# Optimization experiments

Measured on AMD Instinct MI355X. Metric: run time of the kernel, lower is better.

Reference implementation:

```python
import jax, jax.numpy as jnp
import numpy as np

D_STATE = 8
D_CONV = 4
DT_RANK = 8
THRESHOLD = 0.5
KPOOL = 3
PAD = (KPOOL - 1) // 2
EPS = 1e-5


def _rmsnorm(x, w):
    return x * jax.lax.rsqrt(jnp.mean(x * x, axis=-1, keepdims=True) + EPS) * w


def _dw_causal_conv(x, w, b):
    # x: (L, T, C), w: (C, 1, K) depthwise causal conv along T
    xt = jnp.transpose(x, (0, 2, 1))  # (L, C, T)
    y = jax.lax.conv_general_dilated(
        xt, w, window_strides=(1,), padding=[(D_CONV - 1, 0)],
        dimension_numbers=('NCH', 'OIH', 'NCH'), feature_group_count=xt.shape[1])
    return jnp.transpose(y, (0, 2, 1)) + b


def _selective_scan(x, delta, A, B, Cm, D):
    # x, delta: (L,T,d); A: (d,n); B, Cm: (L,T,n); D: (d,)
    dA = jnp.exp(delta[..., None] * A)                        # (L,T,d,n)
    dBx = (delta * x)[..., None] * B[:, :, None, :]           # (L,T,d,n)
    def combine(a, b):
        a1, b1 = a
        a2, b2 = b
        return (a2 * a1, a2 * b1 + b2)
    _, h = jax.lax.associative_scan(combine, (dA, dBx), axis=1)
    y = jnp.einsum('ltdn,ltn->ltd', h, Cm)
    return y + x * D


def _mamba_block(x, in_proj, conv_w, conv_b, x_proj_w, dt_proj_w, dt_proj_b,
                 A_log_f, A_log_b, D_f, D_b, out_proj_w, rms_w):
    # single-depth bidirectional (bimamba-v2 style) block, expand=1, residual + RMSNorm
    res = x
    xn = _rmsnorm(x, rms_w)
    xz = xn @ in_proj                       # (L,T,2C)
    xi, z = jnp.split(xz, 2, axis=-1)
    xi = jax.nn.silu(_dw_causal_conv(xi, conv_w, conv_b))
    dbl = xi @ x_proj_w                     # (L,T,dt_rank+2*d_state)
    dt = dbl[..., :DT_RANK]
    Bm = dbl[..., DT_RANK:DT_RANK + D_STATE]
    Cm = dbl[..., DT_RANK + D_STATE:]
    delta = jax.nn.softplus(dt @ dt_proj_w + dt_proj_b)
    A_f = -jnp.exp(A_log_f)
    A_b = -jnp.exp(A_log_b)
    flip = lambda a: a[:, ::-1]
    y_f = _selective_scan(xi, delta, A_f, Bm, Cm, D_f)
    y_b = flip(_selective_scan(flip(xi), flip(delta), A_b, flip(Bm), flip(Cm), D_b))
    y = 0.5 * (y_f + y_b) * jax.nn.silu(z)  # if_devide_out -> average two directions
    return res + y @ out_proj_w


def reference(feats, in_proj, conv_w, conv_b, x_proj_w, dt_proj_w, dt_proj_b,
              A_log_f, A_log_b, D_f, D_b, out_proj_w, rms_w, mlp_w, mlp_b,
              record_len):
    N, C, H, W = feats.shape
    T = H * W
    rec = np.asarray(record_len)  # static ragged group sizes
    ends = np.cumsum(rec)
    starts = ends - rec
    masks = []
    for s0, L in zip(starts.tolist(), rec.tolist()):
        g = feats[s0:s0 + L]                       # (L,C,H,W)
        if L > 1:
            x = g.reshape(L, C, T).transpose(0, 2, 1)  # l c h w -> l (h w) c
            feat = _mamba_block(x, in_proj, conv_w, conv_b, x_proj_w, dt_proj_w,
                                dt_proj_b, A_log_f, A_log_b, D_f, D_b,
                                out_proj_w, rms_w)
            score = jax.nn.sigmoid(feat @ mlp_w + mlp_b)   # (L,T,1)
            ego = jnp.ones((1, T, 1), feats.dtype)
            bs = jnp.concatenate([ego, score[1:]], axis=0)
        else:
            bs = jnp.ones((1, T, 1), feats.dtype)
        bs = bs.transpose(0, 2, 1).reshape(L, 1, H, W)     # l (h w) c -> l c h w
        masks.append(jnp.where(bs > THRESHOLD, 1.0, 0.0).astype(feats.dtype))
    mask = jnp.concatenate(masks, axis=0)                  # (N,1,H,W)
    pooled = jax.lax.reduce_window(
        mask, -jnp.inf, jax.lax.max,
        window_dimensions=(1, 1, KPOOL, KPOOL), window_strides=(1, 1, 1, 1),
        padding=[(0, 0), (0, 0), (PAD, PAD), (PAD, PAD)])
    return pooled


def setup_inputs():
    key = jax.random.key(0)
    ks = jax.random.split(key, 8)
    C, H, W = 128, 96, 96
    record_len = np.array([2, 3, 1, 2, 4], dtype=np.int64)
    N = int(record_len.sum())
    s = 0.05
    A_log = jnp.log(jnp.broadcast_to(
        jnp.arange(1, D_STATE + 1, dtype=jnp.float32), (C, D_STATE)))
    return {
        'feats': jax.random.normal(ks[0], (N, C, H, W), jnp.float32),
        'in_proj': jax.random.normal(ks[1], (C, 2 * C), jnp.float32) * s,
        'conv_w': jax.random.normal(ks[2], (C, 1, D_CONV), jnp.float32) * s,
        'conv_b': jnp.zeros((C,), jnp.float32),
        'x_proj_w': jax.random.normal(ks[3], (C, DT_RANK + 2 * D_STATE), jnp.float32) * s,
        'dt_proj_w': jax.random.normal(ks[4], (DT_RANK, C), jnp.float32) * s,
        'dt_proj_b': jnp.full((C,), 0.1, jnp.float32),
        'A_log_f': A_log,
        'A_log_b': A_log,
        'D_f': jnp.ones((C,), jnp.float32),
        'D_b': jnp.ones((C,), jnp.float32),
        'out_proj_w': jax.random.normal(ks[5], (C, C), jnp.float32) * s,
        'rms_w': jnp.ones((C,), jnp.float32),
        'mlp_w': jax.random.normal(ks[6], (C, 1), jnp.float32) * s,
        'mlp_b': jnp.zeros((1,), jnp.float32),
        'record_len': jnp.asarray(record_len),
    }
```

## Files before the change

### kernel.cpp

```cpp
#include <hip/hip_runtime.h>
#include <cstdint>
#include <cstddef>

#define C_CH 128
#define T_TOK 9216
#define H_IMG 96
#define W_IMG 96
#define NSTATE 8

#define CHUNK 64
#define RHALO 32
#define REGION (CHUNK + 2 * RHALO)

#define ASTRIDE 68
#define XSTRIDE 129
#define AU_FLOATS 8704

__device__ __forceinline__ float siluf_dev(float x) {
  return x / (1.0f + expf(-x));
}

__device__ __forceinline__ float fast_silu(float x) {
  return __fdividef(x, 1.0f + __expf(-x));
}

__global__ __launch_bounds__(128) void k0_setup(
    const int* __restrict__ rec, int n_groups, int N,
    const float* __restrict__ out_proj_w, const float* __restrict__ mlp_w,
    float* __restrict__ vvec, int* __restrict__ slot)
{
  const int tid = threadIdx.x;
  if (tid == 0) {
    int f = 0, sl = 0;
    for (int g = 0; g < n_groups; ++g) {
      const int L = rec[g];
      slot[f] = -1;
      for (int i = 1; i < L; ++i) slot[f + i] = sl++;
      f += L;
    }
  }
  if (tid < C_CH) {
    float acc = 0.0f;
    for (int j = 0; j < C_CH; ++j) acc += out_proj_w[tid * C_CH + j] * mlp_w[j];
    vvec[tid] = acc;
  }
}

__global__ __launch_bounds__(256, 4) void k12_gemmproj(
    const float* __restrict__ feats, const float* __restrict__ in_proj,
    const float* __restrict__ rms_w, const float* __restrict__ mlp_w,
    const float* __restrict__ mlp_b, const float* __restrict__ vvec,
    const float* __restrict__ conv_w, const float* __restrict__ conv_b,
    const float* __restrict__ x_proj_w,
    const float* __restrict__ dt_proj_w, const float* __restrict__ dt_proj_b,
    const int* __restrict__ slot,
    float* __restrict__ wbuf, float* __restrict__ logit,
    float* __restrict__ xd_g, float* __restrict__ bc_g)
{
  __shared__ float Asm[AU_FLOATS];
  __shared__ float redA[256], redB[256];
  __shared__ float irS[68];
  __shared__ float haloA[12];
  __shared__ float dtb[64 * 8];
  const int f = blockIdx.y;
  const int s = slot[f];
  if (s < 0) return;
  const int m0 = blockIdx.x * 64;
  const int tid = threadIdx.x;
  const size_t rowbase = (size_t)s * T_TOK;

  {
    const int c0 = tid >> 4;
    const int tq = (tid & 15) * 4;
    const float* src = feats + (size_t)f * C_CH * T_TOK + m0 + tq;
    #pragma unroll
    for (int i = 0; i < 8; ++i) {
      const int c = c0 + i * 16;
      const float4 x4 = *(const float4*)(src + (size_t)c * T_TOK);
      *(float4*)&Asm[c * ASTRIDE + 4 + tq] = x4;
    }
  }
  if (m0 > 0 && tid < C_CH) {
    const float* src = feats + (size_t)f * C_CH * T_TOK + (size_t)tid * T_TOK + m0 - 3;
    Asm[tid * ASTRIDE + 0] = src[0];
    Asm[tid * ASTRIDE + 1] = src[1];
    Asm[tid * ASTRIDE + 2] = src[2];
  }
  __syncthreads();
  {
    const int t = tid & 63;
    const int q = tid >> 6;
    float ssum = 0.0f, rm = 0.0f;
    for (int cc = q * 32; cc < q * 32 + 32; ++cc) {
      const float val = Asm[cc * ASTRIDE + 4 + t];
      ssum += val * val;
      rm += val * mlp_w[cc];
    }
    redA[tid] = ssum; redB[tid] = rm;
    if (m0 > 0 && tid < 12) {
      const int j = tid >> 2, qh = tid & 3;
      float ss = 0.0f;
      for (int cc = qh * 32; cc < qh * 32 + 32; ++cc) {
        const float v = Asm[cc * ASTRIDE + j];
        ss += v * v;
      }
      haloA[tid] = ss;
    }
  }
  __syncthreads();
  if (tid < 64) {
    const int t = tid;
    const float ssum = redA[t] + redA[t + 64] + redA[t + 128] + redA[t + 192];
    const float rm   = redB[t] + redB[t + 64] + redB[t + 128] + redB[t + 192];
    const float ir = 1.0f / sqrtf(ssum * (1.0f / C_CH) + 1e-5f);
    logit[rowbase + m0 + t] = rm + mlp_b[0];
    irS[4 + t] = ir;
  } else if (m0 > 0 && tid < 67) {
    const int j = tid - 64;
    const float ss = haloA[j * 4] + haloA[j * 4 + 1] + haloA[j * 4 + 2] + haloA[j * 4 + 3];
    irS[j] = 1.0f / sqrtf(ss * (1.0f / C_CH) + 1e-5f);
  }
  __syncthreads();
  {
    const int t = tid & 63;
    const int q = tid >> 6;
    const float ir = irS[4 + t];
    for (int cc = q * 32; cc < q * 32 + 32; ++cc)
      Asm[cc * ASTRIDE + 4 + t] = (Asm[cc * ASTRIDE + 4 + t] * ir) * rms_w[cc];
    if (m0 > 0 && tid < 12) {
      const int j = tid >> 2, qh = tid & 3;
      const float irh = irS[j];
      for (int cc = qh * 32; cc < qh * 32 + 32; ++cc)
        Asm[cc * ASTRIDE + j] = (Asm[cc * ASTRIDE + j] * irh) * rms_w[cc];
    }
  }
  __syncthreads();

  const int ti = tid >> 4;
  const int tc = tid & 15;

#define GEMM_CHUNK(N0, ACC) do {                                              \
    const float* bp = in_proj + (N0) + tc * 4;                                \
    _Pragma("unroll 8")                                                       \
    for (int k = 0; k < C_CH; ++k) {                                          \
      const float4 a4 = *(const float4*)&Asm[k * ASTRIDE + 4 + ti * 4];       \
      const float4 b4 = *(const float4*)(bp + (size_t)k * 256);               \
      ACC[0][0] += a4.x * b4.x; ACC[0][1] += a4.x * b4.y; ACC[0][2] += a4.x * b4.z; ACC[0][3] += a4.x * b4.w; \
      ACC[1][0] += a4.y * b4.x; ACC[1][1] += a4.y * b4.y; ACC[1][2] += a4.y * b4.z; ACC[1][3] += a4.y * b4.w; \
      ACC[2][0] += a4.z * b4.x; ACC[2][1] += a4.z * b4.y; ACC[2][2] += a4.z * b4.z; ACC[2][3] += a4.z * b4.w; \
      ACC[3][0] += a4.w * b4.x; ACC[3][1] += a4.w * b4.y; ACC[3][2] += a4.w * b4.z; ACC[3][3] += a4.w * b4.w; \
    } } while (0)

  #pragma unroll
  for (int zc4 = 0; zc4 < 2; ++zc4) {
    float acc[4][4];
    #pragma unroll
    for (int i = 0; i < 4; ++i)
      #pragma unroll
      for (int j = 0; j < 4; ++j) acc[i][j] = 0.0f;
    GEMM_CHUNK(128 + zc4 * 64, acc);
    const int zc = zc4 * 64 + tc * 4;
    const float4 v4 = *(const float4*)&vvec[zc];
    #pragma unroll
    for (int i = 0; i < 4; ++i) {
      const int t = m0 + ti * 4 + i;
      float4 o;
      o.x = 0.5f * siluf_dev(acc[i][0]) * v4.x;
      o.y = 0.5f * siluf_dev(acc[i][1]) * v4.y;
      o.z = 0.5f * siluf_dev(acc[i][2]) * v4.z;
      o.w = 0.5f * siluf_dev(acc[i][3]) * v4.w;
      *(float4*)&wbuf[(rowbase + t) * C_CH + zc] = o;
    }
  }

  float acc0[4][4], acc1[4][4];
  #pragma unroll
  for (int i = 0; i < 4; ++i)
    #pragma unroll
    for (int j = 0; j < 4; ++j) { acc0[i][j] = 0.0f; acc1[i][j] = 0.0f; }
  GEMM_CHUNK(0, acc0);
  GEMM_CHUNK(64, acc1);
#undef GEMM_CHUNK

  float hx0 = 0.0f, hx1 = 0.0f;
  {
    const int j0 = tid >> 7;
    const int cc0 = tid & 127;
    if (m0 > 0) {
      for (int k = 0; k < C_CH; ++k) {
        const float b0v = in_proj[(size_t)k * 256 + cc0];
        hx0 += Asm[k * ASTRIDE + j0] * b0v;
        if (tid < 128) hx1 += Asm[k * ASTRIDE + 2] * in_proj[(size_t)k * 256 + tid];
      }
    }
  }
  __syncthreads();

  {
    #pragma unroll
    for (int i = 0; i < 4; ++i) {
      const int row = 3 + ti * 4 + i;
      #pragma unroll
      for (int j = 0; j < 4; ++j) {
        Asm[row * XSTRIDE + tc * 4 + j] = acc0[i][j];
        Asm[row * XSTRIDE + 64 + tc * 4 + j] = acc1[i][j];
      }
    }
    Asm[(tid >> 7) * XSTRIDE + (tid & 127)] = hx0;
    if (tid < 128) Asm[2 * XSTRIDE + tid] = hx1;
  }
  __syncthreads();

  const int c = tid & 127;
  const int half = tid >> 7;
  {
    const float4 cw = *(const float4*)(conv_w + c * 4);
    const float cb = conv_b[c];
    const int row0 = half ? 35 : 3;
    float xm1 = Asm[(row0 - 1) * XSTRIDE + c];
    float xm2 = Asm[(row0 - 2) * XSTRIDE + c];
    float xm3 = Asm[(row0 - 3) * XSTRIDE + c];
    __syncthreads();
    #pragma unroll
    for (int i = 0; i < 32; ++i) {
      const int row = row0 + i;
      const float cur = Asm[row * XSTRIDE + c];
      const float sum = cw.x * xm3 + cw.y * xm2 + cw.z * xm1 + cw.w * cur + cb;
      Asm[row * XSTRIDE + c] = fast_silu(sum);
      xm3 = xm2; xm2 = xm1; xm1 = cur;
    }
  }
  __syncthreads();

  {
    const int q6 = __builtin_amdgcn_readfirstlane(tid >> 6) * 6;
    const int tok = tid & 63;
    float acc[6] = {0, 0, 0, 0, 0, 0};
    for (int cc = 0; cc < C_CH; ++cc) {
      const float xv = Asm[(3 + tok) * XSTRIDE + cc];
      #pragma unroll
      for (int jj = 0; jj < 6; ++jj)
        acc[jj] += xv * x_proj_w[cc * 24 + q6 + jj];
    }
    #pragma unroll
    for (int jj = 0; jj < 6; ++jj) {
      const int o = q6 + jj;
      if (o < 8) dtb[tok * 8 + o] = acc[jj];
      else       bc_g[(rowbase + m0 + tok) * 16 + (o - 8)] = acc[jj];
    }
  }
  __syncthreads();

  {
    float dw[8];
    #pragma unroll
    for (int r = 0; r < 8; ++r) dw[r] = dt_proj_w[r * C_CH + c];
    const float bias = dt_proj_b[c];
    for (int i = 0; i < 32; ++i) {
      const int tok = half * 32 + i;
      const float4 d0 = *(const float4*)&dtb[tok * 8];
      const float4 d1 = *(const float4*)&dtb[tok * 8 + 4];
      float pre = bias;
      pre += d0.x * dw[0] + d0.y * dw[1] + d0.z * dw[2] + d0.w * dw[3];
      pre += d1.x * dw[4] + d1.y * dw[5] + d1.z * dw[6] + d1.w * dw[7];
      const float dlt = fmaxf(pre, 0.0f) + __logf(1.0f + __expf(-fabsf(pre)));
      float2 xd;
      xd.x = Asm[(3 + tok) * XSTRIDE + c];
      xd.y = dlt;
      *(float2*)&xd_g[(rowbase + m0 + tok) * (2 * C_CH) + c * 2] = xd;
    }
  }
}

__global__ __launch_bounds__(256, 4) void k3_scan(
    const float* __restrict__ xd_g, const float* __restrict__ wbuf,
    const float* __restrict__ bc_g,
    const float* __restrict__ A_log_f, const float* __restrict__ A_log_b,
    const float* __restrict__ D_f, const float* __restrict__ D_b,
    const int* __restrict__ slot, float* __restrict__ logit)
{
  __shared__ float bc[REGION * 16];
  const int f = blockIdx.y;
  const int s = slot[f];
  if (s < 0) return;
  const int c0 = blockIdx.x * CHUNK;
  const int r0 = c0 - RHALO;
  const int tid = threadIdx.x;
  const int c = tid & 127;
  const int half = tid >> 7;
  const size_t rowbase = (size_t)s * T_TOK;

  {
    const long grow = ((long)rowbase + r0) * 16;
    const int lo  = (r0 < 0) ? (-r0) * 4 : 0;
    const int hi  = (r0 + REGION > T_TOK) ? (T_TOK - r0) * 4 : REGION * 4;
    #pragma unroll
    for (int i = 0; i < 2; ++i) {
      const int idx = tid + i * 256;
      if (idx >= lo && idx < hi)
        *(float4*)&bc[idx * 4] = *(const float4*)&bc_g[grow + (long)idx * 4];
    }
  }
  __syncthreads();

  float Ac[8];
  const float* Alog = half ? A_log_b : A_log_f;
  #pragma unroll
  for (int n = 0; n < NSTATE; ++n) Ac[n] = -expf(Alog[c * NSTATE + n]);
  const float Dd = half ? D_b[c] : D_f[c];
  float h[8] = {0, 0, 0, 0, 0, 0, 0, 0};

  const float a0 = Ac[0];
  int okl = 1;
  #pragma unroll
  for (int n = 1; n < NSTATE; ++n)
    okl &= (fabsf(Ac[n] - (float)(n + 1) * a0) <= 1e-4f * fabsf(Ac[n])) ? 1 : 0;
  const bool fastA = (__all(okl) != 0);

  auto decay8 = [&](float dlt, float* dA) {
    if (fastA) {
      const float e1 = __expf(dlt * a0);
      const float e2 = e1 * e1, e3 = e2 * e1, e4 = e2 * e2;
      dA[0] = e1; dA[1] = e2; dA[2] = e3; dA[3] = e4;
      dA[4] = e4 * e1; dA[5] = e4 * e2; dA[6] = e4 * e3; dA[7] = e4 * e4;
    } else {
      #pragma unroll
      for (int n = 0; n < NSTATE; ++n) dA[n] = __expf(dlt * Ac[n]);
    }
  };

  if (half == 0) {
    const int tb = (r0 < 0) ? 0 : r0;
    const int outg0 = (c0 - tb) >> 3;
    const int ng = (c0 + CHUNK - tb) >> 3;
    for (int g = 0; g < ng; ++g) {
      const int t0 = tb + g * 8;
      const bool out = (g >= outg0);
      float xg[8], dg[8], wg[8];
      #pragma unroll
      for (int j = 0; j < 8; ++j) {
        const size_t r = rowbase + t0 + j;
        const float2 xd = *(const float2*)&xd_g[r * (2 * C_CH) + c * 2];
        xg[j] = xd.x;
        dg[j] = xd.y;
        wg[j] = out ? wbuf[r * C_CH + c] : 0.0f;
      }
      #pragma unroll
      for (int j = 0; j < 8; ++j) {
        const int t = t0 + j;
        const int p = t - r0;
        const float dlt = dg[j];
        const float xiv = xg[j];
        const float u = dlt * xiv;
        const float4 b0 = *(const float4*)&bc[p * 16];
        const float4 b1 = *(const float4*)&bc[p * 16 + 4];
        float dA[8];
        decay8(dlt, dA);
        h[0] = dA[0] * h[0] + u * b0.x;
        h[1] = dA[1] * h[1] + u * b0.y;
        h[2] = dA[2] * h[2] + u * b0.z;
        h[3] = dA[3] * h[3] + u * b0.w;
        h[4] = dA[4] * h[4] + u * b1.x;
        h[5] = dA[5] * h[5] + u * b1.y;
        h[6] = dA[6] * h[6] + u * b1.z;
        h[7] = dA[7] * h[7] + u * b1.w;
        if (out) {
          const float4 cc0 = *(const float4*)&bc[p * 16 + 8];
          const float4 cc1 = *(const float4*)&bc[p * 16 + 12];
          float y = xiv * Dd;
          y += h[0] * cc0.x + h[1] * cc0.y + h[2] * cc0.z + h[3] * cc0.w;
          y += h[4] * cc1.x + h[5] * cc1.y + h[6] * cc1.z + h[7] * cc1.w;
          float contrib = y * wg[j];
          contrib += __shfl_xor(contrib, 1);
          contrib += __shfl_xor(contrib, 2);
          contrib += __shfl_xor(contrib, 4);
          contrib += __shfl_xor(contrib, 8);
          contrib += __shfl_xor(contrib, 16);
          contrib += __shfl_xor(contrib, 32);
          if ((tid & 63) == 0) atomicAdd(&logit[rowbase + t], contrib);
        }
      }
    }
  } else {
    const int te2e = r0 + REGION;
    const int te2 = (te2e > T_TOK) ? T_TOK : te2e;
    const int outg0 = (te2 - (c0 + CHUNK)) >> 3;
    const int ng = (te2 - c0) >> 3;
    for (int g = 0; g < ng; ++g) {
      const int t0 = te2 - 1 - g * 8;
      const bool out = (g >= outg0);
      float xg[8], dg[8], wg[8];
      #pragma unroll
      for (int j = 0; j < 8; ++j) {
        const size_t r = rowbase + t0 - j;
        const float2 xd = *(const float2*)&xd_g[r * (2 * C_CH) + c * 2];
        xg[j] = xd.x;
        dg[j] = xd.y;
        wg[j] = out ? wbuf[r * C_CH + c] : 0.0f;
      }
      #pragma unroll
      for (int j = 0; j < 8; ++j) {
        const int t = t0 - j;
        const int p = t - r0;
        const float dlt = dg[j];
        const float xiv = xg[j];
        const float u = dlt * xiv;
        const float4 b0 = *(const float4*)&bc[p * 16];
        const float4 b1 = *(const float4*)&bc[p * 16 + 4];
        float dA[8];
        decay8(dlt, dA);
        h[0] = dA[0] * h[0] + u * b0.x;
        h[1] = dA[1] * h[1] + u * b0.y;
        h[2] = dA[2] * h[2] + u * b0.z;
        h[3] = dA[3] * h[3] + u * b0.w;
        h[4] = dA[4] * h[4] + u * b1.x;
        h[5] = dA[5] * h[5] + u * b1.y;
        h[6] = dA[6] * h[6] + u * b1.z;
        h[7] = dA[7] * h[7] + u * b1.w;
        if (out) {
          const float4 cc0 = *(const float4*)&bc[p * 16 + 8];
          const float4 cc1 = *(const float4*)&bc[p * 16 + 12];
          float y = xiv * Dd;
          y += h[0] * cc0.x + h[1] * cc0.y + h[2] * cc0.z + h[3] * cc0.w;
          y += h[4] * cc1.x + h[5] * cc1.y + h[6] * cc1.z + h[7] * cc1.w;
          float contrib = y * wg[j];
          contrib += __shfl_xor(contrib, 1);
          contrib += __shfl_xor(contrib, 2);
          contrib += __shfl_xor(contrib, 4);
          contrib += __shfl_xor(contrib, 8);
          contrib += __shfl_xor(contrib, 16);
          contrib += __shfl_xor(contrib, 32);
          if ((tid & 63) == 0) atomicAdd(&logit[rowbase + t], contrib);
        }
      }
    }
  }
}

__global__ __launch_bounds__(128) void k4_pool(
    const float* __restrict__ logit, const int* __restrict__ slot,
    float* __restrict__ out)
{
  const int w = threadIdx.x;
  if (w >= W_IMG) return;
  const int hh = blockIdx.x;
  const int f = blockIdx.y;
  const int s = slot[f];
  float m = 0.0f;
  if (s < 0) {
    m = 1.0f;
  } else {
    for (int dh = -1; dh <= 1; ++dh) {
      const int h2 = hh + dh;
      if (h2 < 0 || h2 >= H_IMG) continue;
      for (int dw = -1; dw <= 1; ++dw) {
        const int w2 = w + dw;
        if (w2 < 0 || w2 >= W_IMG) continue;
        if (logit[(size_t)s * T_TOK + h2 * W_IMG + w2] > 0.0f) m = 1.0f;
      }
    }
  }
  out[(size_t)f * T_TOK + hh * W_IMG + w] = m;
}

extern "C" void kernel_launch(void* const* d_in, const int* in_sizes, int n_in,
                              void* d_out, int out_size, void* d_ws, size_t ws_size,
                              hipStream_t stream) {
  const float* feats      = (const float*)d_in[0];
  const float* in_proj    = (const float*)d_in[1];
  const float* conv_w     = (const float*)d_in[2];
  const float* conv_b     = (const float*)d_in[3];
  const float* x_proj_w   = (const float*)d_in[4];
  const float* dt_proj_w  = (const float*)d_in[5];
  const float* dt_proj_b  = (const float*)d_in[6];
  const float* A_log_f    = (const float*)d_in[7];
  const float* A_log_b    = (const float*)d_in[8];
  const float* D_f        = (const float*)d_in[9];
  const float* D_b        = (const float*)d_in[10];
  const float* out_proj_w = (const float*)d_in[11];
  const float* rms_w      = (const float*)d_in[12];
  const float* mlp_w      = (const float*)d_in[13];
  const float* mlp_b      = (const float*)d_in[14];
  const int*   rec        = (const int*)d_in[15];

  const int N = in_sizes[0] / (C_CH * T_TOK);
  const int n_groups = in_sizes[15];
  int S = N - n_groups;
  if (S < 1) S = 1;

  char* p = (char*)d_ws;
  float* vvec  = (float*)p; p += 1024;
  int*   slot  = (int*)p;   p += ((N * 4 + 255) / 256) * 256;
  float* logit = (float*)p; p += (size_t)S * T_TOK * 4;
  float* wA    = (float*)p; p += (size_t)S * T_TOK * C_CH * 4;
  float* xd    = (float*)p; p += (size_t)S * T_TOK * (2 * C_CH) * 4;
  float* bcg   = (float*)p; p += (size_t)S * T_TOK * 16 * 4;
  (void)ws_size; (void)n_in; (void)out_size;

  k0_setup<<<1, 128, 0, stream>>>(rec, n_groups, N, out_proj_w, mlp_w, vvec, slot);
  k12_gemmproj<<<dim3(T_TOK / 64, N), 256, 0, stream>>>(
      feats, in_proj, rms_w, mlp_w, mlp_b, vvec,
      conv_w, conv_b, x_proj_w, dt_proj_w, dt_proj_b, slot,
      wA, logit, xd, bcg);
  k3_scan<<<dim3(T_TOK / CHUNK, N), 256, 0, stream>>>(
      xd, wA, bcg, A_log_f, A_log_b, D_f, D_b, slot, logit);
  k4_pool<<<dim3(H_IMG, N), 128, 0, stream>>>(logit, slot, (float*)d_out);
}
```

Baseline: 314.1 us.

## Run in_proj GEMM on bf16 MFMA with three-way split emulating fp32

Replaces the scalar FP32 FMA in_proj GEMM with bf16 MFMA 16x16x32 instructions. Both operands are split into hi/mid/lo bf16 parts, and six cross products are summed to approximate FP32 accuracy. The weights are pre-split and packed into an MFMA-friendly layout by extra blocks in the setup kernel, while activations are split on the fly from shared memory. The cost is six MFMAs per tile, three B-plane global loads, and a different output register mapping for the epilogue.

After: 309.5 us. Within noise of the previous version (-1.5%).

```diff
diff --git a/kernel.cpp b/kernel.cpp
--- a/kernel.cpp
+++ b/kernel.cpp
@@ -16,6 +16,11 @@
 #define XSTRIDE 129
 #define AU_FLOATS 8704
 
+#define BPLANE 32768
+
+typedef __attribute__((ext_vector_type(8))) short short8v;
+typedef __attribute__((ext_vector_type(4))) float f32x4;
+
 __device__ __forceinline__ float siluf_dev(float x) {
   return x / (1.0f + expf(-x));
 }
@@ -24,25 +29,56 @@
   return __fdividef(x, 1.0f + __expf(-x));
 }
 
-__global__ __launch_bounds__(128) void k0_setup(
+__device__ __forceinline__ unsigned short bf16_rne(float x) {
+  unsigned int u = __float_as_uint(x);
+  unsigned int r = u + 0x7FFFu + ((u >> 16) & 1u);
+  return (unsigned short)(r >> 16);
+}
+__device__ __forceinline__ float bf16_tof(unsigned short h) {
+  return __uint_as_float(((unsigned int)h) << 16);
+}
+
+__global__ __launch_bounds__(256) void k0_setup(
     const int* __restrict__ rec, int n_groups, int N,
     const float* __restrict__ out_proj_w, const float* __restrict__ mlp_w,
-    float* __restrict__ vvec, int* __restrict__ slot)
+    const float* __restrict__ in_proj,
+    float* __restrict__ vvec, int* __restrict__ slot,
+    unsigned short* __restrict__ Bpk)
 {
+  const int bid = blockIdx.x;
   const int tid = threadIdx.x;
-  if (tid == 0) {
-    int f = 0, sl = 0;
-    for (int g = 0; g < n_groups; ++g) {
-      const int L = rec[g];
-      slot[f] = -1;
-      for (int i = 1; i < L; ++i) slot[f + i] = sl++;
-      f += L;
-    }
-  }
-  if (tid < C_CH) {
-    float acc = 0.0f;
-    for (int j = 0; j < C_CH; ++j) acc += out_proj_w[tid * C_CH + j] * mlp_w[j];
-    vvec[tid] = acc;
+  if (bid == 0) {
+    if (tid == 0) {
+      int f = 0, sl = 0;
+      for (int g = 0; g < n_groups; ++g) {
+        const int L = rec[g];
+        slot[f] = -1;
+        for (int i = 1; i < L; ++i) slot[f + i] = sl++;
+        f += L;
+      }
+    }
+    if (tid < C_CH) {
+      float acc = 0.0f;
+      for (int j = 0; j < C_CH; ++j) acc += out_proj_w[tid * C_CH + j] * mlp_w[j];
+      vvec[tid] = acc;
+    }
+  } else {
+    const int flat = (bid - 1) * 256 + tid;
+    #pragma unroll
+    for (int e = 0; e < 4; ++e) {
+      const int el = flat * 4 + e;
+      const int k = el >> 8, n = el & 255;
+      const float a = in_proj[el];
+      const unsigned short h = bf16_rne(a);
+      const float r1 = a - bf16_tof(h);
+      const unsigned short md = bf16_rne(r1);
+      const unsigned short lo = bf16_rne(r1 - bf16_tof(md));
+      const int kg = k >> 3, i = k & 7;
+      const size_t base = ((size_t)kg * 256 + n) * 8 + i;
+      Bpk[base] = h;
+      Bpk[BPLANE + base] = md;
+      Bpk[2 * BPLANE + base] = lo;
+    }
   }
 }
 
@@ -53,7 +89,7 @@
     const float* __restrict__ conv_w, const float* __restrict__ conv_b,
     const float* __restrict__ x_proj_w,
     const float* __restrict__ dt_proj_w, const float* __restrict__ dt_proj_b,
-    const int* __restrict__ slot,
+    const int* __restrict__ slot, const unsigned short* __restrict__ Bpk,
     float* __restrict__ wbuf, float* __restrict__ logit,
     float* __restrict__ xd_g, float* __restrict__ bc_g)
 {
@@ -136,51 +172,55 @@
   }
   __syncthreads();
 
-  const int ti = tid >> 4;
-  const int tc = tid & 15;
-
-#define GEMM_CHUNK(N0, ACC) do {                                              \
-    const float* bp = in_proj + (N0) + tc * 4;                                \
-    _Pragma("unroll 8")                                                       \
-    for (int k = 0; k < C_CH; ++k) {                                          \
-      const float4 a4 = *(const float4*)&Asm[k * ASTRIDE + 4 + ti * 4];       \
-      const float4 b4 = *(const float4*)(bp + (size_t)k * 256);               \
-      ACC[0][0] += a4.x * b4.x; ACC[0][1] += a4.x * b4.y; ACC[0][2] += a4.x * b4.z; ACC[0][3] += a4.x * b4.w; \
-      ACC[1][0] += a4.y * b4.x; ACC[1][1] += a4.y * b4.y; ACC[1][2] += a4.y * b4.z; ACC[1][3] += a4.y * b4.w; \
-      ACC[2][0] += a4.z * b4.x; ACC[2][1] += a4.z * b4.y; ACC[2][2] += a4.z * b4.z; ACC[2][3] += a4.z * b4.w; \
-      ACC[3][0] += a4.w * b4.x; ACC[3][1] += a4.w * b4.y; ACC[3][2] += a4.w * b4.z; ACC[3][3] += a4.w * b4.w; \
-    } } while (0)
-
+  const int wv = tid >> 6;
+  const int l  = tid & 63;
+  const int ln = l & 15;
+  const int kg = l >> 4;
+  const int drow0 = kg * 4;
+
+  f32x4 acc[16];
   #pragma unroll
-  for (int zc4 = 0; zc4 < 2; ++zc4) {
-    float acc[4][4];
-    #pragma unroll
-    for (int i = 0; i < 4; ++i)
-      #pragma unroll
-      for (int j = 0; j < 4; ++j) acc[i][j] = 0.0f;
-    GEMM_CHUNK(128 + zc4 * 64, acc);
-    const int zc = zc4 * 64 + tc * 4;
-    const float4 v4 = *(const float4*)&vvec[zc];
-    #pragma unroll
-    for (int i = 0; i < 4; ++i) {
-      const int t = m0 + ti * 4 + i;
-      float4 o;
-      o.x = 0.5f * siluf_dev(acc[i][0]) * v4.x;
-      o.y = 0.5f * siluf_dev(acc[i][1]) * v4.y;
-      o.z = 0.5f * siluf_dev(acc[i][2]) * v4.z;
-      o.w = 0.5f * siluf_dev(acc[i][3]) * v4.w;
-      *(float4*)&wbuf[(rowbase + t) * C_CH + zc] = o;
-    }
-  }
-
-  float acc0[4][4], acc1[4][4];
+  for (int t = 0; t < 16; ++t) acc[t] = (f32x4){0.f, 0.f, 0.f, 0.f};
+
   #pragma unroll
-  for (int i = 0; i < 4; ++i)
-    #pragma unroll
-    for (int j = 0; j < 4; ++j) { acc0[i][j] = 0.0f; acc1[i][j] = 0.0f; }
-  GEMM_CHUNK(0, acc0);
-  GEMM_CHUNK(64, acc1);
-#undef GEMM_CHUNK
+  for (int q = 0; q < 4; ++q) {
+    short8v Ah, Am, Al;
+    #pragma unroll
+    for (int i = 0; i < 8; ++i) {
+      const int k = 32 * q + kg * 8 + i;
+      const float a = Asm[k * ASTRIDE + 4 + 16 * wv + ln];
+      const unsigned short h = bf16_rne(a);
+      const float r1 = a - bf16_tof(h);
+      const unsigned short md = bf16_rne(r1);
+      const unsigned short lo = bf16_rne(r1 - bf16_tof(md));
+      Ah[i] = (short)h; Am[i] = (short)md; Al[i] = (short)lo;
+    }
+    const unsigned short* bq = Bpk + ((size_t)(4 * q + kg) * 256 + ln) * 8;
+    #pragma unroll
+    for (int t = 0; t < 16; ++t) {
+      const unsigned short* bp = bq + (size_t)t * 128;
+      const short8v Bh = *(const short8v*)(bp);
+      const short8v Bm = *(const short8v*)(bp + BPLANE);
+      const short8v Bl = *(const short8v*)(bp + 2 * BPLANE);
+      acc[t] = __builtin_amdgcn_mfma_f32_16x16x32_bf16(Ah, Bh, acc[t], 0, 0, 0);
+      acc[t] = __builtin_amdgcn_mfma_f32_16x16x32_bf16(Ah, Bm, acc[t], 0, 0, 0);
+      acc[t] = __builtin_amdgcn_mfma_f32_16x16x32_bf16(Am, Bh, acc[t], 0, 0, 0);
+      acc[t] = __builtin_amdgcn_mfma_f32_16x16x32_bf16(Ah, Bl, acc[t], 0, 0, 0);
+      acc[t] = __builtin_amdgcn_mfma_f32_16x16x32_bf16(Am, Bm, acc[t], 0, 0, 0);
+      acc[t] = __builtin_amdgcn_mfma_f32_16x16x32_bf16(Al, Bh, acc[t], 0, 0, 0);
+    }
+  }
+
+  #pragma unroll
+  for (int t = 8; t < 16; ++t) {
+    const int ch = (t - 8) * 16 + ln;
+    const float v = vvec[ch];
+    #pragma unroll
+    for (int r = 0; r < 4; ++r) {
+      const int tok = m0 + 16 * wv + drow0 + r;
+      wbuf[(rowbase + tok) * C_CH + ch] = 0.5f * siluf_dev(acc[t][r]) * v;
+    }
+  }
 
   float hx0 = 0.0f, hx1 = 0.0f;
   {
@@ -198,12 +238,12 @@
 
   {
     #pragma unroll
-    for (int i = 0; i < 4; ++i) {
-      const int row = 3 + ti * 4 + i;
-      #pragma unroll
-      for (int j = 0; j < 4; ++j) {
-        Asm[row * XSTRIDE + tc * 4 + j] = acc0[i][j];
-        Asm[row * XSTRIDE + 64 + tc * 4 + j] = acc1[i][j];
+    for (int t = 0; t < 8; ++t) {
+      const int ch = t * 16 + ln;
+      #pragma unroll
+      for (int r = 0; r < 4; ++r) {
+        const int row = 3 + 16 * wv + drow0 + r;
+        Asm[row * XSTRIDE + ch] = acc[t][r];
       }
     }
     Asm[(tid >> 7) * XSTRIDE + (tid & 127)] = hx0;
@@ -235,18 +275,18 @@
   {
     const int q6 = __builtin_amdgcn_readfirstlane(tid >> 6) * 6;
     const int tok = tid & 63;
-    float acc[6] = {0, 0, 0, 0, 0, 0};
+    float acp[6] = {0, 0, 0, 0, 0, 0};
     for (int cc = 0; cc < C_CH; ++cc) {
       const float xv = Asm[(3 + tok) * XSTRIDE + cc];
       #pragma unroll
       for (int jj = 0; jj < 6; ++jj)
-        acc[jj] += xv * x_proj_w[cc * 24 + q6 + jj];
+        acp[jj] += xv * x_proj_w[cc * 24 + q6 + jj];
     }
     #pragma unroll
     for (int jj = 0; jj < 6; ++jj) {
       const int o = q6 + jj;
-      if (o < 8) dtb[tok * 8 + o] = acc[jj];
-      else       bc_g[(rowbase + m0 + tok) * 16 + (o - 8)] = acc[jj];
+      if (o < 8) dtb[tok * 8 + o] = acp[jj];
+      else       bc_g[(rowbase + m0 + tok) * 16 + (o - 8)] = acp[jj];
     }
   }
   __syncthreads();
@@ -491,16 +531,18 @@
   char* p = (char*)d_ws;
   float* vvec  = (float*)p; p += 1024;
   int*   slot  = (int*)p;   p += ((N * 4 + 255) / 256) * 256;
+  unsigned short* Bpk = (unsigned short*)p; p += 3 * BPLANE * 2;
   float* logit = (float*)p; p += (size_t)S * T_TOK * 4;
   float* wA    = (float*)p; p += (size_t)S * T_TOK * C_CH * 4;
   float* xd    = (float*)p; p += (size_t)S * T_TOK * (2 * C_CH) * 4;
   float* bcg   = (float*)p; p += (size_t)S * T_TOK * 16 * 4;
   (void)ws_size; (void)n_in; (void)out_size;
 
-  k0_setup<<<1, 128, 0, stream>>>(rec, n_groups, N, out_proj_w, mlp_w, vvec, slot);
+  k0_setup<<<33, 256, 0, stream>>>(rec, n_groups, N, out_proj_w, mlp_w, in_proj,
+                                   vvec, slot, Bpk);
   k12_gemmproj<<<dim3(T_TOK / 64, N), 256, 0, stream>>>(
       feats, in_proj, rms_w, mlp_w, mlp_b, vvec,
-      conv_w, conv_b, x_proj_w, dt_proj_w, dt_proj_b, slot,
+      conv_w, conv_b, x_proj_w, dt_proj_w, dt_proj_b, slot, Bpk,
       wA, logit, xd, bcg);
   k3_scan<<<dim3(T_TOK / CHUNK, N), 256, 0, stream>>>(
       xd, wA, bcg, A_log_f, A_log_b, D_f, D_b, slot, logit);
```
